# Kernel optimization log

Measured on AMD Instinct MI355X. Metric: run time of the kernel, lower is better.

The kernel has to match this reference:

```python
import jax, jax.numpy as jnp
import numpy as np


def setup_inputs() -> dict:
    key = jax.random.key(0)
    k1, k2, k3, k4 = jax.random.split(key, 4)
    B, Lq, Lk, d = 8, 2048, 2048, 64
    queries = jax.random.normal(k1, (B, Lq, d), dtype=jnp.float32)
    keys = jax.random.normal(k2, (B, Lk, d), dtype=jnp.float32)
    values = jax.random.normal(k3, (B, Lk, d), dtype=jnp.float32)
    valid_lens = jax.random.randint(k4, (B,), 0, 2048, dtype=jnp.int64)
    return {"queries": queries, "keys": keys, "values": values, "valid_lens": valid_lens}


def reference(queries, keys, values, valid_lens):
    # scores: [B, Lq, Lk]
    d = queries.shape[-1]
    scale = 1.0 / jnp.sqrt(jnp.asarray(d, dtype=queries.dtype))
    scores = jnp.einsum("bqd,bkd->bqk", queries, keys) * scale
    # length mask: key positions >= valid_len[b] get -1e6 (as in sequence_mask)
    Lk = keys.shape[1]
    mask = jnp.arange(Lk)[None, None, :] < valid_lens[:, None, None]  # [B,1,Lk]
    scores = jnp.where(mask, scores, jnp.asarray(-1e6, dtype=scores.dtype))
    attn = jax.nn.softmax(scores, axis=-1)
    # dropout p=0.0 -> identity
    return jnp.einsum("bqk,bkd->bqd", attn, values)
```

## Files before the change

kernel.cpp:

```cpp
#include <hip/hip_runtime.h>
#include <hip/hip_bf16.h>
#include <math.h>

typedef __attribute__((ext_vector_type(8))) short short8;
typedef __attribute__((ext_vector_type(16))) float f32x16;

#define DHEAD 64
#define KVB 32
#define QB 32
#define NW 8
#define NWF 4

__device__ __forceinline__ unsigned pack2_bf16(float a, float b) {
  unsigned ua = __builtin_bit_cast(unsigned, a);
  unsigned ub = __builtin_bit_cast(unsigned, b);
  ua = (ua + 0x7fffu + ((ua >> 16) & 1u)) >> 16;
  ub = (ub + 0x7fffu + ((ub >> 16) & 1u)) >> 16;
  return (ua & 0xffffu) | (ub << 16);
}

union Frag { unsigned u[4]; short8 s; };

__global__ __launch_bounds__(256)
void prep_f(const float* __restrict__ Q, const float* __restrict__ K,
            const float* __restrict__ V, unsigned short* __restrict__ Qf,
            unsigned short* __restrict__ Kf, unsigned short* __restrict__ Vf,
            int Lq, int Lk) {
  __shared__ float Vs[32][65];
  const int b = blockIdx.y, t = blockIdx.x, tid = threadIdx.x;
  const int LkT = Lk / 32, LqT = Lq / 32;
  const int kk = tid >> 6, lane = tid & 63;
  const int row = lane & 31, colb = kk * 16 + ((lane >> 5) & 1) * 8;
  const float cQ = 0.125f * 1.4426950408889634f;

  if (t < LqT) {
    const float* src = Q + (((size_t)b * Lq + t * 32 + row) * DHEAD + colb);
    Frag fr;
    #pragma unroll
    for (int j = 0; j < 4; ++j)
      fr.u[j] = pack2_bf16(src[2 * j] * cQ, src[2 * j + 1] * cQ);
    *(short8*)(Qf + ((size_t)(b * LqT + t)) * 2048 + tid * 8) = fr.s;
  }
  if (t < LkT) {
    const float* src = K + (((size_t)b * Lk + t * 32 + row) * DHEAD + colb);
    Frag fr;
    #pragma unroll
    for (int j = 0; j < 4; ++j)
      fr.u[j] = pack2_bf16(src[2 * j], src[2 * j + 1]);
    *(short8*)(Kf + ((size_t)(b * LkT + t)) * 2048 + tid * 8) = fr.s;

    const size_t vbase = ((size_t)b * Lk + t * 32) * DHEAD;
    for (int e = tid; e < 32 * DHEAD; e += 256) Vs[e >> 6][e & 63] = V[vbase + e];
    __syncthreads();
    const int region = tid >> 6;
    const int vkk = region & 1, half = region >> 1;
    const int krow = vkk * 16 + ((lane >> 5) & 1) * 8;
    const int d = half * 32 + (lane & 31);
    Frag fv;
    #pragma unroll
    for (int j = 0; j < 4; ++j)
      fv.u[j] = pack2_bf16(Vs[krow + 2 * j][d], Vs[krow + 2 * j + 1][d]);
    *(short8*)(Vf + ((size_t)(b * LkT + t)) * 2048 + tid * 8) = fv.s;
  }
}

__device__ __forceinline__ void tile_body(
    int t, int nkb, int vl, int lane, int hi,
    const unsigned short* __restrict__ kb, const unsigned short* __restrict__ vb,
    const short8 (&qf)[4], short8 (&kc)[4], short8 (&kn)[4],
    f32x16& o0, f32x16& o1, float& m, float& l) {
  const float MASKV = -1442695.04f;

  const unsigned short* vt = vb + (size_t)t * 2048;
  short8 vf0[2], vf1[2];
  #pragma unroll
  for (int kk = 0; kk < 2; ++kk) {
    vf0[kk] = *(const short8*)(vt + kk * 512 + lane * 8);
    vf1[kk] = *(const short8*)(vt + (2 + kk) * 512 + lane * 8);
  }

  f32x16 s = {};
  #pragma unroll
  for (int kk = 0; kk < 4; ++kk)
    s = __builtin_amdgcn_mfma_f32_32x32x16_bf16(kc[kk], qf[kk], s, 0, 0, 0);

  const int tn = t + NW;
  if (tn < nkb) {
    const unsigned short* ktn = kb + (size_t)tn * 2048;
    #pragma unroll
    for (int kk = 0; kk < 4; ++kk)
      kn[kk] = *(const short8*)(ktn + kk * 512 + lane * 8);
  }

  const int key0 = t * KVB;
  if (key0 + KVB > vl) {
    #pragma unroll
    for (int r = 0; r < 16; ++r) {
      const int key = key0 + (r & 3) + 8 * (r >> 2) + 4 * hi;
      if (key >= vl) s[r] = MASKV;
    }
  }

  float t0 = fmaxf(s[0], s[1]),  t1 = fmaxf(s[2], s[3]);
  float t2 = fmaxf(s[4], s[5]),  t3 = fmaxf(s[6], s[7]);
  float t4 = fmaxf(s[8], s[9]),  t5 = fmaxf(s[10], s[11]);
  float t6 = fmaxf(s[12], s[13]), t7 = fmaxf(s[14], s[15]);
  t0 = fmaxf(t0, t1); t2 = fmaxf(t2, t3); t4 = fmaxf(t4, t5); t6 = fmaxf(t6, t7);
  t0 = fmaxf(t0, t2); t4 = fmaxf(t4, t6);
  float tm = fmaxf(t0, t4);
  tm = fmaxf(tm, __shfl_xor(tm, 32));

  if (__any(tm > m)) {
    const float mnew  = fmaxf(m, tm);
    const float alpha = exp2f(m - mnew);
    #pragma unroll
    for (int r = 0; r < 16; ++r) { o0[r] *= alpha; o1[r] *= alpha; }
    l *= alpha;
    m = mnew;
  }
  #pragma unroll
  for (int r = 0; r < 16; ++r) s[r] = exp2f(s[r] - m);
  float u0 = s[0] + s[1],  u1 = s[2] + s[3];
  float u2 = s[4] + s[5],  u3 = s[6] + s[7];
  float u4 = s[8] + s[9],  u5 = s[10] + s[11];
  float u6 = s[12] + s[13], u7 = s[14] + s[15];
  u0 += u1; u2 += u3; u4 += u5; u6 += u7; u0 += u2; u4 += u6;
  l += u0 + u4 + __shfl_xor(u0 + u4, 32);

  short8 pf[2];
  #pragma unroll
  for (int kk = 0; kk < 2; ++kk) {
    const unsigned A0 = pack2_bf16(s[8 * kk + 0], s[8 * kk + 1]);
    const unsigned B0 = pack2_bf16(s[8 * kk + 2], s[8 * kk + 3]);
    const unsigned C0 = pack2_bf16(s[8 * kk + 4], s[8 * kk + 5]);
    const unsigned D0 = pack2_bf16(s[8 * kk + 6], s[8 * kk + 7]);
    const unsigned sA = (unsigned)__shfl_xor((int)A0, 32);
    const unsigned sB = (unsigned)__shfl_xor((int)B0, 32);
    const unsigned sC = (unsigned)__shfl_xor((int)C0, 32);
    const unsigned sD = (unsigned)__shfl_xor((int)D0, 32);
    Frag fr;
    fr.u[0] = hi ? sC : A0;
    fr.u[1] = hi ? sD : B0;
    fr.u[2] = hi ? C0 : sA;
    fr.u[3] = hi ? D0 : sB;
    pf[kk] = fr.s;
  }

  #pragma unroll
  for (int kk = 0; kk < 2; ++kk) {
    o0 = __builtin_amdgcn_mfma_f32_32x32x16_bf16(vf0[kk], pf[kk], o0, 0, 0, 0);
    o1 = __builtin_amdgcn_mfma_f32_32x32x16_bf16(vf1[kk], pf[kk], o1, 0, 0, 0);
  }
}

__global__ __launch_bounds__(NW * 64, 2)
void fa8(const unsigned short* __restrict__ Qf, const unsigned short* __restrict__ Kf,
         const unsigned short* __restrict__ Vf, const int* __restrict__ VL,
         float* __restrict__ Og, int Lq, int Lk, int nqt) {
  __shared__ float OLs[4][QB][DHEAD + 1];
  __shared__ float mL[4][QB];
  __shared__ float lL[4][QB];
  __shared__ float FIN[QB][DHEAD + 2];

  const int tid  = threadIdx.x;
  const int w    = tid >> 6;
  const int lane = tid & 63;
  const int l31  = lane & 31;
  const int hi   = lane >> 5;
  const int qt   = blockIdx.x;
  const int b    = blockIdx.y;
  const int vl   = VL[b];

  const int LkT = Lk / KVB;
  int nkb = (vl == 0) ? LkT : ((vl + KVB - 1) / KVB);
  if (nkb > LkT) nkb = LkT;

  const unsigned short* qtile = Qf + ((size_t)(b * nqt + qt)) * 2048;
  short8 qf[4];
  #pragma unroll
  for (int kk = 0; kk < 4; ++kk)
    qf[kk] = *(const short8*)(qtile + kk * 512 + lane * 8);

  const unsigned short* kb = Kf + (size_t)b * LkT * 2048;
  const unsigned short* vb = Vf + (size_t)b * LkT * 2048;

  f32x16 o0 = {};
  f32x16 o1 = {};
  float m = -INFINITY;
  float l = 0.0f;

  int t = w;
  if (t < nkb) {
    short8 kA[4], kB[4];
    const unsigned short* kt = kb + (size_t)t * 2048;
    #pragma unroll
    for (int kk = 0; kk < 4; ++kk)
      kA[kk] = *(const short8*)(kt + kk * 512 + lane * 8);
    while (true) {
      tile_body(t, nkb, vl, lane, hi, kb, vb, qf, kA, kB, o0, o1, m, l);
      t += NW; if (t >= nkb) break;
      tile_body(t, nkb, vl, lane, hi, kb, vb, qf, kB, kA, o0, o1, m, l);
      t += NW; if (t >= nkb) break;
    }
  }

  #pragma unroll
  for (int ph = 0; ph < 3; ++ph) {
    const int wlo  = (ph == 0) ? 4 : (ph == 1) ? 2 : 1;
    const int wcnt = wlo == 1 ? 1 : wlo;

    if (w >= wlo && w < wlo + wcnt) {
      const int s = w - wlo;
      if (hi == 0) { mL[s][l31] = m; lL[s][l31] = l; }
      #pragma unroll
      for (int r = 0; r < 16; ++r) {
        const int dr = (r & 3) + 8 * (r >> 2) + 4 * hi;
        OLs[s][l31][dr]      = o0[r];
        OLs[s][l31][dr + 32] = o1[r];
      }
    }
    __syncthreads();
    if (w < wcnt) {
      const int s = w;
      const float m2 = mL[s][l31];
      const float l2 = lL[s][l31];
      const float M  = fmaxf(m, m2);
      const float a  = (l  > 0.f) ? exp2f(m - M)  : 0.f;
      const float a2 = (l2 > 0.f) ? exp2f(m2 - M) : 0.f;
      #pragma unroll
      for (int r = 0; r < 16; ++r) {
        const int dr = (r & 3) + 8 * (r >> 2) + 4 * hi;
        o0[r] = o0[r] * a + OLs[s][l31][dr]      * a2;
        o1[r] = o1[r] * a + OLs[s][l31][dr + 32] * a2;
      }
      l = l * a + l2 * a2;
      m = M;
    }
    __syncthreads();
  }

  if (w == 0) {
    const float rl = (l > 0.f) ? 1.0f / l : 0.0f;
    #pragma unroll
    for (int r = 0; r < 16; ++r) {
      const int dr = (r & 3) + 8 * (r >> 2) + 4 * hi;
      FIN[l31][dr]      = o0[r] * rl;
      FIN[l31][dr + 32] = o1[r] * rl;
    }
  }
  __syncthreads();
  const size_t base = ((size_t)b * Lq + (size_t)qt * QB) * DHEAD;
  for (int e = tid; e < QB * DHEAD; e += NW * 64)
    Og[base + e] = FIN[e >> 6][e & 63];
}

__global__ __launch_bounds__(NWF * 64)
void fa_fwd(const float* __restrict__ Qg, const float* __restrict__ Kg,
            const float* __restrict__ Vg, const int* __restrict__ VL,
            float* __restrict__ Og, int Lq, int Lk) {
  __shared__ float OLs[NWF][QB][DHEAD + 1];
  __shared__ float mLs[NWF][QB];
  __shared__ float lLs[NWF][QB];

  const int tid  = threadIdx.x;
  const int w    = tid >> 6;
  const int lane = tid & 63;
  const int l31  = lane & 31;
  const int hi   = lane >> 5;
  const int q0   = blockIdx.x * QB;
  const int b    = blockIdx.y;
  const int vl   = VL[b];

  const float* Qb = Qg + (size_t)b * Lq * DHEAD;
  const float* Kb = Kg + (size_t)b * Lk * DHEAD;
  const float* Vb = Vg + (size_t)b * Lk * DHEAD;

  const float cQ = 0.125f * 1.4426950408889634f;
  short8 qf[4];
  {
    const float* qrow = Qb + (size_t)(q0 + l31) * DHEAD + hi * 8;
    #pragma unroll
    for (int kk = 0; kk < 4; ++kk) {
      Frag fr;
      #pragma unroll
      for (int j = 0; j < 4; ++j)
        fr.u[j] = pack2_bf16(qrow[kk * 16 + 2 * j] * cQ,
                             qrow[kk * 16 + 2 * j + 1] * cQ);
      qf[kk] = fr.s;
    }
  }

  f32x16 o0 = {};
  f32x16 o1 = {};
  float m = -INFINITY;
  float l = 0.0f;

  int nkb = (vl == 0) ? (Lk / KVB) : ((vl + KVB - 1) / KVB);
  if (nkb > Lk / KVB) nkb = Lk / KVB;
  const int nt = (nkb > w) ? ((nkb - w + NWF - 1) / NWF) : 0;

  const float MASKV = -1442695.04f;

  float kraw[32], vraw[32];

  if (nt > 0) {
    const float* krow = Kb + (size_t)(w * KVB + l31) * DHEAD + hi * 8;
    #pragma unroll
    for (int kk = 0; kk < 4; ++kk)
      #pragma unroll
      for (int j = 0; j < 8; ++j) kraw[kk * 8 + j] = krow[kk * 16 + j];
  }

  for (int t = 0; t < nt; ++t) {
    const int key0 = (w + t * NWF) * KVB;

    short8 kf[4];
    #pragma unroll
    for (int kk = 0; kk < 4; ++kk) {
      Frag fr;
      #pragma unroll
      for (int j = 0; j < 4; ++j)
        fr.u[j] = pack2_bf16(kraw[kk * 8 + 2 * j], kraw[kk * 8 + 2 * j + 1]);
      kf[kk] = fr.s;
    }

    #pragma unroll
    for (int kk = 0; kk < 2; ++kk) {
      const float* vrow = Vb + (size_t)(key0 + kk * 16 + hi * 8) * DHEAD + l31;
      #pragma unroll
      for (int j = 0; j < 8; ++j) {
        vraw[kk * 16 + j]     = vrow[j * DHEAD];
        vraw[kk * 16 + 8 + j] = vrow[j * DHEAD + 32];
      }
    }

    f32x16 s = {};
    #pragma unroll
    for (int kk = 0; kk < 4; ++kk)
      s = __builtin_amdgcn_mfma_f32_32x32x16_bf16(kf[kk], qf[kk], s, 0, 0, 0);

    if (t + 1 < nt) {
      const float* krow = Kb + (size_t)(key0 + NWF * KVB + l31) * DHEAD + hi * 8;
      #pragma unroll
      for (int kk = 0; kk < 4; ++kk)
        #pragma unroll
        for (int j = 0; j < 8; ++j) kraw[kk * 8 + j] = krow[kk * 16 + j];
    }

    if (key0 + KVB > vl) {
      #pragma unroll
      for (int r = 0; r < 16; ++r) {
        const int key = key0 + (r & 3) + 8 * (r >> 2) + 4 * hi;
        if (key >= vl) s[r] = MASKV;
      }
    }

    float t0 = fmaxf(s[0], s[1]),  t1 = fmaxf(s[2], s[3]);
    float t2 = fmaxf(s[4], s[5]),  t3 = fmaxf(s[6], s[7]);
    float t4 = fmaxf(s[8], s[9]),  t5 = fmaxf(s[10], s[11]);
    float t6 = fmaxf(s[12], s[13]), t7 = fmaxf(s[14], s[15]);
    t0 = fmaxf(t0, t1); t2 = fmaxf(t2, t3); t4 = fmaxf(t4, t5); t6 = fmaxf(t6, t7);
    t0 = fmaxf(t0, t2); t4 = fmaxf(t4, t6);
    float tm = fmaxf(t0, t4);
    tm = fmaxf(tm, __shfl_xor(tm, 32));
    const float mnew  = fmaxf(m, tm);
    const float alpha = exp2f(m - mnew);
    #pragma unroll
    for (int r = 0; r < 16; ++r) s[r] = exp2f(s[r] - mnew);
    float u0 = s[0] + s[1],  u1 = s[2] + s[3];
    float u2 = s[4] + s[5],  u3 = s[6] + s[7];
    float u4 = s[8] + s[9],  u5 = s[10] + s[11];
    float u6 = s[12] + s[13], u7 = s[14] + s[15];
    u0 += u1; u2 += u3; u4 += u5; u6 += u7; u0 += u2; u4 += u6;
    float sum = u0 + u4;
    sum += __shfl_xor(sum, 32);
    l = l * alpha + sum;
    m = mnew;
    #pragma unroll
    for (int r = 0; r < 16; ++r) { o0[r] *= alpha; o1[r] *= alpha; }

    short8 pf[2];
    #pragma unroll
    for (int kk = 0; kk < 2; ++kk) {
      const unsigned A0 = pack2_bf16(s[8 * kk + 0], s[8 * kk + 1]);
      const unsigned B0 = pack2_bf16(s[8 * kk + 2], s[8 * kk + 3]);
      const unsigned C0 = pack2_bf16(s[8 * kk + 4], s[8 * kk + 5]);
      const unsigned D0 = pack2_bf16(s[8 * kk + 6], s[8 * kk + 7]);
      const unsigned sA = (unsigned)__shfl_xor((int)A0, 32);
      const unsigned sB = (unsigned)__shfl_xor((int)B0, 32);
      const unsigned sC = (unsigned)__shfl_xor((int)C0, 32);
      const unsigned sD = (unsigned)__shfl_xor((int)D0, 32);
      Frag fr;
      fr.u[0] = hi ? sC : A0;
      fr.u[1] = hi ? sD : B0;
      fr.u[2] = hi ? C0 : sA;
      fr.u[3] = hi ? D0 : sB;
      pf[kk] = fr.s;
    }

    #pragma unroll
    for (int kk = 0; kk < 2; ++kk) {
      Frag f0, f1;
      #pragma unroll
      for (int j = 0; j < 4; ++j) {
        f0.u[j] = pack2_bf16(vraw[kk * 16 + 2 * j],     vraw[kk * 16 + 2 * j + 1]);
        f1.u[j] = pack2_bf16(vraw[kk * 16 + 8 + 2 * j], vraw[kk * 16 + 8 + 2 * j + 1]);
      }
      o0 = __builtin_amdgcn_mfma_f32_32x32x16_bf16(f0.s, pf[kk], o0, 0, 0, 0);
      o1 = __builtin_amdgcn_mfma_f32_32x32x16_bf16(f1.s, pf[kk], o1, 0, 0, 0);
    }
  }

  if (hi == 0) { mLs[w][l31] = m; lLs[w][l31] = l; }
  #pragma unroll
  for (int r = 0; r < 16; ++r) {
    const int dr = (r & 3) + 8 * (r >> 2) + 4 * hi;
    OLs[w][l31][dr]      = o0[r];
    OLs[w][l31][dr + 32] = o1[r];
  }
  __syncthreads();

  for (int e = tid; e < QB * DHEAD; e += NWF * 64) {
    const int q = e >> 6;
    const int d = e & 63;
    float M = mLs[0][q];
    #pragma unroll
    for (int ww = 1; ww < NWF; ++ww) M = fmaxf(M, mLs[ww][q]);
    float L = 0.f, acc = 0.f;
    #pragma unroll
    for (int ww = 0; ww < NWF; ++ww) {
      const float wgt = exp2f(mLs[ww][q] - M);
      L   += lLs[ww][q] * wgt;
      acc += OLs[ww][q][d] * wgt;
    }
    Og[((size_t)b * Lq + q0 + q) * DHEAD + d] = acc / L;
  }
}

extern "C" void kernel_launch(void* const* d_in, const int* in_sizes, int n_in,
                              void* d_out, int out_size, void* d_ws, size_t ws_size,
                              hipStream_t stream) {
  const float* Q  = (const float*)d_in[0];
  const float* K  = (const float*)d_in[1];
  const float* V  = (const float*)d_in[2];
  const int*   VL = (const int*)d_in[3];
  float* O = (float*)d_out;

  const int B  = in_sizes[3];
  const int Lq = in_sizes[0] / (B * DHEAD);
  const int Lk = in_sizes[1] / (B * DHEAD);
  const int nqt = Lq / QB;

  const size_t qfE = (size_t)B * Lq * DHEAD;
  const size_t kfE = (size_t)B * Lk * DHEAD;
  const size_t need = (qfE + kfE * 2) * 2;

  if (ws_size >= need) {
    unsigned short* Qf = (unsigned short*)d_ws;
    unsigned short* Kf = Qf + qfE;
    unsigned short* Vf = Kf + kfE;

    const int maxT = (Lq > Lk ? Lq : Lk) / 32;
    dim3 pgrid(maxT, B);
    prep_f<<<pgrid, 256, 0, stream>>>(Q, K, V, Qf, Kf, Vf, Lq, Lk);
    dim3 g1(nqt, B);
    fa8<<<g1, NW * 64, 0, stream>>>(Qf, Kf, Vf, VL, O, Lq, Lk, nqt);
  } else {
    dim3 grid(Lq / QB, B);
    fa_fwd<<<grid, NWF * 64, 0, stream>>>(Q, K, V, VL, O, Lq, Lk);
  }
}
```

Before: 33.41 us.

## Fuse Q conversion into attention kernel, skip masked KV prep, prefetch V

Drops the Q bf16 pre-pass and converts and scales Q in registers inside the attention kernel, removing a workspace write and read. The K/V prep kernel now exits early for tiles beyond the valid length, so masked-out keys are never converted. V tiles are double-buffered in registers alongside K, loaded one iteration ahead, and MFMA blocks are wrapped in s_setprio to favour matrix issue. This raises register pressure and adds strided fp32 Q loads per block.

```diff
diff --git a/kernel.cpp b/kernel.cpp
--- a/kernel.cpp
+++ b/kernel.cpp
@@ -22,74 +22,66 @@
 union Frag { unsigned u[4]; short8 s; };
 
 __global__ __launch_bounds__(256)
-void prep_f(const float* __restrict__ Q, const float* __restrict__ K,
-            const float* __restrict__ V, unsigned short* __restrict__ Qf,
-            unsigned short* __restrict__ Kf, unsigned short* __restrict__ Vf,
-            int Lq, int Lk) {
+void prep_kv(const float* __restrict__ K, const float* __restrict__ V,
+             unsigned short* __restrict__ Kf, unsigned short* __restrict__ Vf,
+             const int* __restrict__ VL, int Lk) {
   __shared__ float Vs[32][65];
   const int b = blockIdx.y, t = blockIdx.x, tid = threadIdx.x;
-  const int LkT = Lk / 32, LqT = Lq / 32;
+  const int LkT = Lk / 32;
+  const int vl = VL[b];
+  int nkb = (vl == 0) ? LkT : ((vl + 31) / 32);
+  if (nkb > LkT) nkb = LkT;
+  if (t >= nkb) return;
+
   const int kk = tid >> 6, lane = tid & 63;
   const int row = lane & 31, colb = kk * 16 + ((lane >> 5) & 1) * 8;
-  const float cQ = 0.125f * 1.4426950408889634f;
-
-  if (t < LqT) {
-    const float* src = Q + (((size_t)b * Lq + t * 32 + row) * DHEAD + colb);
-    Frag fr;
-    #pragma unroll
-    for (int j = 0; j < 4; ++j)
-      fr.u[j] = pack2_bf16(src[2 * j] * cQ, src[2 * j + 1] * cQ);
-    *(short8*)(Qf + ((size_t)(b * LqT + t)) * 2048 + tid * 8) = fr.s;
-  }
-  if (t < LkT) {
-    const float* src = K + (((size_t)b * Lk + t * 32 + row) * DHEAD + colb);
+  const size_t base = ((size_t)b * Lk + t * 32) * DHEAD;
+
+  {
+    const float* src = K + base + (size_t)row * DHEAD + colb;
     Frag fr;
     #pragma unroll
     for (int j = 0; j < 4; ++j)
       fr.u[j] = pack2_bf16(src[2 * j], src[2 * j + 1]);
     *(short8*)(Kf + ((size_t)(b * LkT + t)) * 2048 + tid * 8) = fr.s;
-
-    const size_t vbase = ((size_t)b * Lk + t * 32) * DHEAD;
-    for (int e = tid; e < 32 * DHEAD; e += 256) Vs[e >> 6][e & 63] = V[vbase + e];
-    __syncthreads();
-    const int region = tid >> 6;
-    const int vkk = region & 1, half = region >> 1;
-    const int krow = vkk * 16 + ((lane >> 5) & 1) * 8;
-    const int d = half * 32 + (lane & 31);
-    Frag fv;
-    #pragma unroll
-    for (int j = 0; j < 4; ++j)
-      fv.u[j] = pack2_bf16(Vs[krow + 2 * j][d], Vs[krow + 2 * j + 1][d]);
-    *(short8*)(Vf + ((size_t)(b * LkT + t)) * 2048 + tid * 8) = fv.s;
-  }
+  }
+  for (int e = tid; e < 32 * DHEAD; e += 256) Vs[e >> 6][e & 63] = V[base + e];
+  __syncthreads();
+  const int region = tid >> 6;
+  const int vkk = region & 1, half = region >> 1;
+  const int krow = vkk * 16 + ((lane >> 5) & 1) * 8;
+  const int d = half * 32 + (lane & 31);
+  Frag fv;
+  #pragma unroll
+  for (int j = 0; j < 4; ++j)
+    fv.u[j] = pack2_bf16(Vs[krow + 2 * j][d], Vs[krow + 2 * j + 1][d]);
+  *(short8*)(Vf + ((size_t)(b * LkT + t)) * 2048 + tid * 8) = fv.s;
 }
 
 __device__ __forceinline__ void tile_body(
     int t, int nkb, int vl, int lane, int hi,
     const unsigned short* __restrict__ kb, const unsigned short* __restrict__ vb,
     const short8 (&qf)[4], short8 (&kc)[4], short8 (&kn)[4],
+    short8 (&vc)[4], short8 (&vn)[4],
     f32x16& o0, f32x16& o1, float& m, float& l) {
   const float MASKV = -1442695.04f;
 
-  const unsigned short* vt = vb + (size_t)t * 2048;
-  short8 vf0[2], vf1[2];
-  #pragma unroll
-  for (int kk = 0; kk < 2; ++kk) {
-    vf0[kk] = *(const short8*)(vt + kk * 512 + lane * 8);
-    vf1[kk] = *(const short8*)(vt + (2 + kk) * 512 + lane * 8);
-  }
-
   f32x16 s = {};
+  __builtin_amdgcn_s_setprio(1);
   #pragma unroll
   for (int kk = 0; kk < 4; ++kk)
     s = __builtin_amdgcn_mfma_f32_32x32x16_bf16(kc[kk], qf[kk], s, 0, 0, 0);
+  __builtin_amdgcn_s_setprio(0);
 
   const int tn = t + NW;
   if (tn < nkb) {
     const unsigned short* ktn = kb + (size_t)tn * 2048;
-    #pragma unroll
-    for (int kk = 0; kk < 4; ++kk)
+    const unsigned short* vtn = vb + (size_t)tn * 2048;
+    #pragma unroll
+    for (int kk = 0; kk < 4; ++kk) {
       kn[kk] = *(const short8*)(ktn + kk * 512 + lane * 8);
+      vn[kk] = *(const short8*)(vtn + kk * 512 + lane * 8);
+    }
   }
 
   const int key0 = t * KVB;
@@ -146,15 +138,16 @@
     pf[kk] = fr.s;
   }
 
-  #pragma unroll
-  for (int kk = 0; kk < 2; ++kk) {
-    o0 = __builtin_amdgcn_mfma_f32_32x32x16_bf16(vf0[kk], pf[kk], o0, 0, 0, 0);
-    o1 = __builtin_amdgcn_mfma_f32_32x32x16_bf16(vf1[kk], pf[kk], o1, 0, 0, 0);
-  }
+  __builtin_amdgcn_s_setprio(1);
+  o0 = __builtin_amdgcn_mfma_f32_32x32x16_bf16(vc[0], pf[0], o0, 0, 0, 0);
+  o1 = __builtin_amdgcn_mfma_f32_32x32x16_bf16(vc[2], pf[0], o1, 0, 0, 0);
+  o0 = __builtin_amdgcn_mfma_f32_32x32x16_bf16(vc[1], pf[1], o0, 0, 0, 0);
+  o1 = __builtin_amdgcn_mfma_f32_32x32x16_bf16(vc[3], pf[1], o1, 0, 0, 0);
+  __builtin_amdgcn_s_setprio(0);
 }
 
 __global__ __launch_bounds__(NW * 64, 2)
-void fa8(const unsigned short* __restrict__ Qf, const unsigned short* __restrict__ Kf,
+void fa8(const float* __restrict__ Qg, const unsigned short* __restrict__ Kf,
          const unsigned short* __restrict__ Vf, const int* __restrict__ VL,
          float* __restrict__ Og, int Lq, int Lk, int nqt) {
   __shared__ float OLs[4][QB][DHEAD + 1];
@@ -175,11 +168,20 @@
   int nkb = (vl == 0) ? LkT : ((vl + KVB - 1) / KVB);
   if (nkb > LkT) nkb = LkT;
 
-  const unsigned short* qtile = Qf + ((size_t)(b * nqt + qt)) * 2048;
+  const float cQ = 0.125f * 1.4426950408889634f;
   short8 qf[4];
-  #pragma unroll
-  for (int kk = 0; kk < 4; ++kk)
-    qf[kk] = *(const short8*)(qtile + kk * 512 + lane * 8);
+  {
+    const float* qrow = Qg + ((size_t)b * Lq + qt * QB + l31) * DHEAD + hi * 8;
+    #pragma unroll
+    for (int kk = 0; kk < 4; ++kk) {
+      Frag fr;
+      #pragma unroll
+      for (int j = 0; j < 4; ++j)
+        fr.u[j] = pack2_bf16(qrow[kk * 16 + 2 * j] * cQ,
+                             qrow[kk * 16 + 2 * j + 1] * cQ);
+      qf[kk] = fr.s;
+    }
+  }
 
   const unsigned short* kb = Kf + (size_t)b * LkT * 2048;
   const unsigned short* vb = Vf + (size_t)b * LkT * 2048;
@@ -191,15 +193,18 @@
 
   int t = w;
   if (t < nkb) {
-    short8 kA[4], kB[4];
+    short8 kA[4], kB[4], vA[4], vB[4];
     const unsigned short* kt = kb + (size_t)t * 2048;
-    #pragma unroll
-    for (int kk = 0; kk < 4; ++kk)
+    const unsigned short* vt = vb + (size_t)t * 2048;
+    #pragma unroll
+    for (int kk = 0; kk < 4; ++kk) {
       kA[kk] = *(const short8*)(kt + kk * 512 + lane * 8);
+      vA[kk] = *(const short8*)(vt + kk * 512 + lane * 8);
+    }
     while (true) {
-      tile_body(t, nkb, vl, lane, hi, kb, vb, qf, kA, kB, o0, o1, m, l);
+      tile_body(t, nkb, vl, lane, hi, kb, vb, qf, kA, kB, vA, vB, o0, o1, m, l);
       t += NW; if (t >= nkb) break;
-      tile_body(t, nkb, vl, lane, hi, kb, vb, qf, kB, kA, o0, o1, m, l);
+      tile_body(t, nkb, vl, lane, hi, kb, vb, qf, kB, kA, vB, vA, o0, o1, m, l);
       t += NW; if (t >= nkb) break;
     }
   }
@@ -451,20 +456,17 @@
   const int Lk = in_sizes[1] / (B * DHEAD);
   const int nqt = Lq / QB;
 
-  const size_t qfE = (size_t)B * Lq * DHEAD;
   const size_t kfE = (size_t)B * Lk * DHEAD;
-  const size_t need = (qfE + kfE * 2) * 2;
+  const size_t need = kfE * 2 * 2;
 
   if (ws_size >= need) {
-    unsigned short* Qf = (unsigned short*)d_ws;
-    unsigned short* Kf = Qf + qfE;
+    unsigned short* Kf = (unsigned short*)d_ws;
     unsigned short* Vf = Kf + kfE;
 
-    const int maxT = (Lq > Lk ? Lq : Lk) / 32;
-    dim3 pgrid(maxT, B);
-    prep_f<<<pgrid, 256, 0, stream>>>(Q, K, V, Qf, Kf, Vf, Lq, Lk);
+    dim3 pgrid(Lk / 32, B);
+    prep_kv<<<pgrid, 256, 0, stream>>>(K, V, Kf, Vf, VL, Lk);
     dim3 g1(nqt, B);
-    fa8<<<g1, NW * 64, 0, stream>>>(Qf, Kf, Vf, VL, O, Lq, Lk, nqt);
+    fa8<<<g1, NW * 64, 0, stream>>>(Q, Kf, Vf, VL, O, Lq, Lk, nqt);
   } else {
     dim3 grid(Lq / QB, B);
     fa_fwd<<<grid, NWF * 64, 0, stream>>>(Q, K, V, VL, O, Lq, Lk);
```

Result: slower. 34.88 us (+4.4%).
